# Performance work log

Hardware: AMD Instinct MI355X
Metric: run time of the kernel (lower is better)

The kernel has to match this reference:

```python
import jax, jax.numpy as jnp
import numpy as np

INPUT_DIM = 1024
NUM_HEADS = 16
D_K = 1024
HEAD_DIM = D_K // NUM_HEADS


def setup_inputs() -> dict:
    key = jax.random.key(0)
    ks = jax.random.split(key, 9)
    s_in = 1.0 / np.sqrt(INPUT_DIM)
    s_dk = 1.0 / np.sqrt(D_K)
    return {
        "x": jax.random.normal(ks[0], (2, 2048, INPUT_DIM), dtype=jnp.float32),
        "Wq": jax.random.uniform(ks[1], (INPUT_DIM, D_K), minval=-s_in, maxval=s_in, dtype=jnp.float32),
        "bq": jax.random.uniform(ks[2], (D_K,), minval=-s_in, maxval=s_in, dtype=jnp.float32),
        "Wk": jax.random.uniform(ks[3], (INPUT_DIM, D_K), minval=-s_in, maxval=s_in, dtype=jnp.float32),
        "bk": jax.random.uniform(ks[4], (D_K,), minval=-s_in, maxval=s_in, dtype=jnp.float32),
        "Wv": jax.random.uniform(ks[5], (INPUT_DIM, D_K), minval=-s_in, maxval=s_in, dtype=jnp.float32),
        "bv": jax.random.uniform(ks[6], (D_K,), minval=-s_in, maxval=s_in, dtype=jnp.float32),
        "Wo": jax.random.uniform(ks[7], (D_K, INPUT_DIM), minval=-s_dk, maxval=s_dk, dtype=jnp.float32),
        "bo": jax.random.uniform(ks[8], (INPUT_DIM,), minval=-s_dk, maxval=s_dk, dtype=jnp.float32),
    }


def reference(x, Wq, bq, Wk, bk, Wv, bv, Wo, bo):
    B, S, _ = x.shape
    H, D = NUM_HEADS, HEAD_DIM
    # QKV projections -> [B, H, S, D]
    q = (x @ Wq + bq).reshape(B, S, H, D).transpose(0, 2, 1, 3)
    k = (x @ Wk + bk).reshape(B, S, H, D).transpose(0, 2, 1, 3)
    v = (x @ Wv + bv).reshape(B, S, H, D).transpose(0, 2, 1, 3)
    scores = jnp.einsum("bhsd,bhtd->bhst", q, k) / jnp.sqrt(jnp.asarray(D, x.dtype))
    attn = jax.nn.softmax(scores, axis=-1)
    out = jnp.einsum("bhst,bhtd->bhsd", attn, v)  # [B,H,S,D]
    out = out.transpose(0, 2, 1, 3).reshape(B, S, H * D)
    return out @ Wo + bo
```

## Files before the change

### kernel.cpp

```cpp
#include <hip/hip_runtime.h>
#include <stdint.h>

typedef _Float16 f16;
typedef f16 f16x4 __attribute__((ext_vector_type(4)));
typedef f16 f16x8 __attribute__((ext_vector_type(8)));
typedef float f32x4 __attribute__((ext_vector_type(4)));
typedef float f32x16 __attribute__((ext_vector_type(16)));

#define AS1 __attribute__((address_space(1)))
#define AS3 __attribute__((address_space(3)))

__device__ __forceinline__ void gll16(const void* g, void* l) {
  __builtin_amdgcn_global_load_lds((AS1 void*)g, (AS3 void*)l, 16, 0, 0);
}

__device__ __forceinline__ f32x4 mfma16(f16x8 a, f16x8 b, f32x4 c) {
  return __builtin_amdgcn_mfma_f32_16x16x32_f16(a, b, c, 0, 0, 0);
}
__device__ __forceinline__ f32x16 mfma32(f16x8 a, f16x8 b, f32x16 c) {
  return __builtin_amdgcn_mfma_f32_32x32x16_f16(a, b, c, 0, 0, 0);
}

__device__ __forceinline__ uint32_t pk_rtn(float a, float b) {
  union { f16 h[2]; uint32_t u; } c;
  c.h[0] = (f16)a;
  c.h[1] = (f16)b;
  return c.u;
}

__device__ __forceinline__ void pl32(uint32_t& x, uint32_t& y) {
  asm("v_permlane32_swap_b32 %0, %1" : "+v"(x), "+v"(y));
}

__device__ __forceinline__ f16x8 mk_bfrag(float e0, float e1, float e2, float e3,
                                          float e4, float e5, float e6, float e7) {
  uint32_t x0 = pk_rtn(e0, e1), y0 = pk_rtn(e4, e5);
  uint32_t x1 = pk_rtn(e2, e3), y1 = pk_rtn(e6, e7);
  pl32(x0, y0);
  pl32(x1, y1);
  union { uint32_t w[4]; f16x8 v; } u;
  u.w[0] = x0; u.w[1] = x1; u.w[2] = y0; u.w[3] = y1;
  return u.v;
}

__device__ __forceinline__ f32x16 zero16() {
  f32x16 z;
#pragma unroll
  for (int i = 0; i < 16; i++) z[i] = 0.f;
  return z;
}


__global__ __launch_bounds__(256) void pack_x_k(const float* __restrict__ x,
                                                f16* __restrict__ xh, int n) {
  int i = (blockIdx.x * 256 + threadIdx.x) * 8;
  if (i < n) {
    float4 a = *(const float4*)(x + i);
    float4 b = *(const float4*)(x + i + 4);
    f16x8 o;
    o[0] = (f16)a.x; o[1] = (f16)a.y; o[2] = (f16)a.z; o[3] = (f16)a.w;
    o[4] = (f16)b.x; o[5] = (f16)b.y; o[6] = (f16)b.z; o[7] = (f16)b.w;
    *(f16x8*)(xh + i) = o;
  }
}

__global__ __launch_bounds__(256) void pack_w_k(const float* __restrict__ Wq,
                                                const float* __restrict__ Wk,
                                                const float* __restrict__ Wv,
                                                const float* __restrict__ Wo,
                                                f16* __restrict__ Wt) {
  __shared__ f16 t[64][65];
  const float* W = (blockIdx.z == 0) ? Wq : (blockIdx.z == 1) ? Wk
                   : (blockIdx.z == 2) ? Wv : Wo;
  int n0 = blockIdx.x * 64, k0 = blockIdx.y * 64;
  int tid = threadIdx.x;
  int kr = tid >> 4;
  int nc = (tid & 15) * 4;
#pragma unroll
  for (int i = 0; i < 4; i++) {
    int k = k0 + kr + i * 16;
    float4 w = *(const float4*)(W + (size_t)k * 1024 + n0 + nc);
    t[nc + 0][kr + i * 16] = (f16)w.x;
    t[nc + 1][kr + i * 16] = (f16)w.y;
    t[nc + 2][kr + i * 16] = (f16)w.z;
    t[nc + 3][kr + i * 16] = (f16)w.w;
  }
  __syncthreads();
  int nr = tid >> 2;
  int c0 = (tid & 3) * 16;
  alignas(16) f16 tmp[16];
#pragma unroll
  for (int e = 0; e < 16; e++) tmp[e] = t[nr][c0 + e];
  f16* dst = Wt + (size_t)(blockIdx.z * 1024 + n0 + nr) * 1024 + k0 + c0;
  *(f16x8*)(dst) = *(const f16x8*)(tmp);
  *(f16x8*)(dst + 8) = *(const f16x8*)(tmp + 8);
}

__device__ __forceinline__ void gemm_main(const f16* __restrict__ A,
                                          const f16* __restrict__ B,
                                          int m0, int n0,
                                          f16* Al, f16* Bl,
                                          f32x4 acc[4][4]) {
  const int K = 1024;
  int tid = threadIdx.x;
  int lane = tid & 63, wid = tid >> 6;
  int wr = (wid >> 1) * 64, wc = (wid & 1) * 64;
#pragma unroll
  for (int mi = 0; mi < 4; mi++)
#pragma unroll
    for (int nj = 0; nj < 4; nj++) {
      f32x4 z = {0.f, 0.f, 0.f, 0.f};
      acc[mi][nj] = z;
    }
  int srow = lane >> 3;
  int sgr = (lane & 7) ^ srow;
  int lr = lane & 15, lg = lane >> 4;
  for (int kt = 0; kt < 16; ++kt) {
    __syncthreads();
#pragma unroll
    for (int q = 0; q < 4; q++) {
      int chunk = wid * 4 + q;
      int row = chunk * 8 + srow;
      gll16(A + (size_t)(m0 + row) * K + kt * 64 + sgr * 8, Al + chunk * 512);
      gll16(B + (size_t)(n0 + row) * K + kt * 64 + sgr * 8, Bl + chunk * 512);
    }
    __syncthreads();
#pragma unroll
    for (int kk = 0; kk < 2; kk++) {
      f16x8 af[4], bf[4];
#pragma unroll
      for (int mi = 0; mi < 4; mi++) {
        int row = wr + mi * 16 + lr;
        int gr = (kk * 4 + lg) ^ (row & 7);
        af[mi] = *(const f16x8*)(Al + row * 64 + gr * 8);
      }
#pragma unroll
      for (int nj = 0; nj < 4; nj++) {
        int row = wc + nj * 16 + lr;
        int gr = (kk * 4 + lg) ^ (row & 7);
        bf[nj] = *(const f16x8*)(Bl + row * 64 + gr * 8);
      }
#pragma unroll
      for (int mi = 0; mi < 4; mi++)
#pragma unroll
        for (int nj = 0; nj < 4; nj++)
          acc[mi][nj] = mfma16(af[mi], bf[nj], acc[mi][nj]);
    }
  }
}

__global__ __launch_bounds__(256) void gemm_qkv_k(const f16* __restrict__ Xh,
                                                  const f16* __restrict__ Wt,
                                                  const float* __restrict__ bq,
                                                  const float* __restrict__ bk,
                                                  const float* __restrict__ bv,
                                                  f16* __restrict__ Q,
                                                  f16* __restrict__ Kb,
                                                  f16* __restrict__ Vt) {
  __shared__ f16 Al[128 * 64];
  __shared__ f16 Bl[128 * 64];
  f32x4 acc[4][4];
  int m0 = blockIdx.y * 128, n0 = blockIdx.x * 128;
  gemm_main(Xh, Wt, m0, n0, Al, Bl, acc);

  int lane = threadIdx.x & 63, wid = threadIdx.x >> 6;
  int wr = (wid >> 1) * 64, wc = (wid & 1) * 64;
  int lg = lane >> 4, lc = lane & 15;
  int which = n0 >> 10;
  if (which == 2) {
#pragma unroll
    for (int mi = 0; mi < 4; mi++)
#pragma unroll
      for (int nj = 0; nj < 4; nj++) {
        int nh = (n0 + wc + nj * 16 + lc) & 1023;
        int h = nh >> 6, d = nh & 63;
        float bb = bv[nh];
        int mbase = m0 + wr + mi * 16 + lg * 4;
        int b = mbase >> 11, s = mbase & 2047;
        f16x4 vv;
#pragma unroll
        for (int r = 0; r < 4; r++) vv[r] = (f16)(acc[mi][nj][r] + bb);
        *(f16x4*)(Vt + ((size_t)(b * 16 + h) * 64 + d) * 2048 + s) = vv;
      }
  } else {
    const float* bias = (which == 0) ? bq : bk;
    f16* out = (which == 0) ? Q : Kb;
    float scale = (which == 0) ? 0.1803368801111204f : 1.0f;
#pragma unroll
    for (int mi = 0; mi < 4; mi++)
#pragma unroll
      for (int nj = 0; nj < 4; nj++) {
        int nh = (n0 + wc + nj * 16 + lc) & 1023;
        int h = nh >> 6, d = nh & 63;
        float bb = bias[nh];
#pragma unroll
        for (int r = 0; r < 4; r++) {
          int m = m0 + wr + mi * 16 + lg * 4 + r;
          int b = m >> 11, s = m & 2047;
          float v = (acc[mi][nj][r] + bb) * scale;
          out[((size_t)(b * 16 + h) * 2048 + s) * 64 + d] = (f16)v;
        }
      }
  }
}

__global__ __launch_bounds__(256) void gemm_out_k(const f16* __restrict__ Oh,
                                                  const f16* __restrict__ Wt,
                                                  const float* __restrict__ bo,
                                                  float* __restrict__ out) {
  __shared__ f16 Al[128 * 64];
  __shared__ f16 Bl[64 * 64];
  const int K = 1024;
  int tid = threadIdx.x, lane = tid & 63, wid = tid >> 6;
  int wr = (wid >> 1) * 64, wc = (wid & 1) * 32;
  f32x4 acc[4][2];
#pragma unroll
  for (int mi = 0; mi < 4; mi++)
#pragma unroll
    for (int nj = 0; nj < 2; nj++) {
      f32x4 z = {0.f, 0.f, 0.f, 0.f};
      acc[mi][nj] = z;
    }
  int m0 = blockIdx.y * 128, n0 = blockIdx.x * 64;
  int srow = lane >> 3, sgr = (lane & 7) ^ srow;
  int lr = lane & 15, lg = lane >> 4;
  for (int kt = 0; kt < 16; ++kt) {
    __syncthreads();
#pragma unroll
    for (int q = 0; q < 4; q++) {
      int chunk = wid * 4 + q;
      int row = chunk * 8 + srow;
      gll16(Oh + (size_t)(m0 + row) * K + kt * 64 + sgr * 8, Al + chunk * 512);
    }
#pragma unroll
    for (int q = 0; q < 2; q++) {
      int chunk = wid * 2 + q;
      int row = chunk * 8 + srow;
      gll16(Wt + (size_t)(n0 + row) * K + kt * 64 + sgr * 8, Bl + chunk * 512);
    }
    __syncthreads();
#pragma unroll
    for (int kk = 0; kk < 2; kk++) {
      f16x8 af[4], bf[2];
#pragma unroll
      for (int mi = 0; mi < 4; mi++) {
        int row = wr + mi * 16 + lr;
        int gr = (kk * 4 + lg) ^ (row & 7);
        af[mi] = *(const f16x8*)(Al + row * 64 + gr * 8);
      }
#pragma unroll
      for (int nj = 0; nj < 2; nj++) {
        int row = wc + nj * 16 + lr;
        int gr = (kk * 4 + lg) ^ (row & 7);
        bf[nj] = *(const f16x8*)(Bl + row * 64 + gr * 8);
      }
#pragma unroll
      for (int mi = 0; mi < 4; mi++)
#pragma unroll
        for (int nj = 0; nj < 2; nj++)
          acc[mi][nj] = mfma16(af[mi], bf[nj], acc[mi][nj]);
    }
  }
  int lg4 = lg * 4, lc = lane & 15;
#pragma unroll
  for (int mi = 0; mi < 4; mi++)
#pragma unroll
    for (int nj = 0; nj < 2; nj++) {
      int n = n0 + wc + nj * 16 + lc;
      float bb = bo[n];
#pragma unroll
      for (int r = 0; r < 4; r++) {
        int m = m0 + wr + mi * 16 + lg4 + r;
        out[(size_t)m * 1024 + n] = acc[mi][nj][r] + bb;
      }
    }
}

__global__ __launch_bounds__(256, 4) void attn_k(const f16* __restrict__ Q,
                                                 const f16* __restrict__ K,
                                                 const f16* __restrict__ Vt,
                                                 f16* __restrict__ Oh) {
  __shared__ alignas(16) char lds_raw[32768];
  f16* Kl = (f16*)lds_raw;
  f16* Vl = (f16*)(lds_raw + 16384);

  int tid = threadIdx.x, lane = tid & 63, wid = tid >> 6;
  int q5 = lane & 31, hi = lane >> 5;
  int qc2 = wid >> 1, hv = wid & 1;
  int b0 = blockIdx.x;
  int qc = (b0 >> 3) & 31;
  int bh = (b0 & 7) + ((b0 >> 8) << 3);
  int q0w = qc * 64 + qc2 * 32;

  const f16* Qp = Q + (size_t)bh * 2048 * 64;
  const f16* Kp = K + (size_t)bh * 2048 * 64;
  const f16* Vp = Vt + (size_t)bh * 64 * 2048;

  f16x8 qf[4];
  {
    const f16* qr = Qp + (size_t)(q0w + q5) * 64 + hi * 8;
#pragma unroll
    for (int ks = 0; ks < 4; ks++) qf[ks] = *(const f16x8*)(qr + ks * 16);
  }

  const f32x16 Z = zero16();
  f16x8 ones;
#pragma unroll
  for (int i = 0; i < 8; i++) ones[i] = (f16)1.0f;

  f32x16 o0 = Z, o1 = Z, osum = Z;

  int srow8 = lane >> 3, swz8 = ((lane & 7) ^ srow8) * 8;
  int ch0 = wid * 2;
  const f16* sK = Kp + (size_t)(ch0 * 8 + srow8) * 64 + swz8;
  const f16* sV = Vp + (size_t)(ch0 * 8 + srow8) * 2048 + swz8;

  auto STAGE = [&](int buf, int t) {
    const f16* k = sK + (size_t)t * 4096;
    const f16* v = sV + t * 64;
    f16* dk = Kl + buf * 4096 + ch0 * 512;
    f16* dv = Vl + buf * 4096 + ch0 * 512;
    gll16(k, dk);
    gll16(k + 8 * 64, dk + 512);
    gll16(v, dv);
    gll16(v + (size_t)8 * 2048, dv + 512);
  };

  int kqoff[4];
#pragma unroll
  for (int ks = 0; ks < 4; ks++)
    kqoff[ks] = (hv * 32 + q5) * 64 + (((2 * ks + hi) ^ (q5 & 7)) << 3);
  int r0 = q5, r1 = q5 + 32;
  int voff0[2], voff1[2];
#pragma unroll
  for (int ks = 0; ks < 2; ks++) {
    voff0[ks] = r0 * 64 + (((hv * 4 + 2 * ks + hi) ^ (r0 & 7)) << 3);
    voff1[ks] = r1 * 64 + (((hv * 4 + 2 * ks + hi) ^ (r1 & 7)) << 3);
  }

  STAGE(0, 0);

  for (int t = 0; t < 32; ++t) {
    int cur = t & 1;
    asm volatile("s_waitcnt vmcnt(0)" ::: "memory");
    __builtin_amdgcn_s_barrier();
    if (t < 31) STAGE(cur ^ 1, t + 1);

    const f16* kb = Kl + cur * 4096;
    const f16* vb = Vl + cur * 4096;

    __builtin_amdgcn_s_setprio(1);
    f32x16 s = mfma32(*(const f16x8*)(kb + kqoff[0]), qf[0], Z);
    s = mfma32(*(const f16x8*)(kb + kqoff[1]), qf[1], s);
    s = mfma32(*(const f16x8*)(kb + kqoff[2]), qf[2], s);
    s = mfma32(*(const f16x8*)(kb + kqoff[3]), qf[3], s);
    __builtin_amdgcn_s_setprio(0);

    f16x8 vf0[2], vf1[2];
#pragma unroll
    for (int ks = 0; ks < 2; ks++) {
      vf0[ks] = *(const f16x8*)(vb + voff0[ks]);
      vf1[ks] = *(const f16x8*)(vb + voff1[ks]);
    }

#pragma unroll
    for (int i = 0; i < 16; i++) s[i] = __builtin_amdgcn_exp2f(s[i]);

    f16x8 pb0 = mk_bfrag(s[0], s[1], s[2], s[3], s[4], s[5], s[6], s[7]);
    f16x8 pb1 = mk_bfrag(s[8], s[9], s[10], s[11], s[12], s[13], s[14], s[15]);

    __builtin_amdgcn_s_setprio(1);
    o0 = mfma32(vf0[0], pb0, o0);
    o0 = mfma32(vf0[1], pb1, o0);
    o1 = mfma32(vf1[0], pb0, o1);
    o1 = mfma32(vf1[1], pb1, o1);
    osum = mfma32(ones, pb0, osum);
    osum = mfma32(ones, pb1, osum);
    __builtin_amdgcn_s_setprio(0);
  }

  float lsum = osum[0];

  __syncthreads();
  float* Ox = (float*)lds_raw + qc2 * (32 * 68);
  float* ml = (float*)lds_raw + 2 * (32 * 68) + qc2 * 32;
  if (hv == 1) {
#pragma unroll
    for (int g = 0; g < 4; g++) {
      f32x4 a, b;
#pragma unroll
      for (int j = 0; j < 4; j++) { a[j] = o0[4 * g + j]; b[j] = o1[4 * g + j]; }
      *(f32x4*)(Ox + q5 * 68 + 8 * g + 4 * hi) = a;
      *(f32x4*)(Ox + q5 * 68 + 32 + 8 * g + 4 * hi) = b;
    }
    if (hi == 0) ml[q5] = lsum;
  }
  __syncthreads();
  if (hv == 0) {
    float inv = 1.f / (lsum + ml[q5]);
    int bB = bh >> 4, hh = bh & 15;
    f16* op = Oh + ((size_t)(bB * 2048 + q0w + q5)) * 1024 + hh * 64;
#pragma unroll
    for (int g = 0; g < 4; g++) {
      f32x4 x0 = *(const f32x4*)(Ox + q5 * 68 + 8 * g + 4 * hi);
      f32x4 x1 = *(const f32x4*)(Ox + q5 * 68 + 32 + 8 * g + 4 * hi);
      f16x4 y0, y1;
#pragma unroll
      for (int j = 0; j < 4; j++) {
        y0[j] = (f16)((o0[4 * g + j] + x0[j]) * inv);
        y1[j] = (f16)((o1[4 * g + j] + x1[j]) * inv);
      }
      int d0 = 8 * g + 4 * hi;
      *(f16x4*)(op + d0) = y0;
      *(f16x4*)(op + 32 + d0) = y1;
    }
  }
}


extern "C" void kernel_launch(void* const* d_in, const int* in_sizes, int n_in,
                              void* d_out, int out_size, void* d_ws, size_t ws_size,
                              hipStream_t stream) {
  const float* x  = (const float*)d_in[0];
  const float* Wq = (const float*)d_in[1];
  const float* bq = (const float*)d_in[2];
  const float* Wk = (const float*)d_in[3];
  const float* bk = (const float*)d_in[4];
  const float* Wv = (const float*)d_in[5];
  const float* bv = (const float*)d_in[6];
  const float* Wo = (const float*)d_in[7];
  const float* bo = (const float*)d_in[8];
  float* out = (float*)d_out;

  char* ws = (char*)d_ws;
  const size_t MB8 = (size_t)8 << 20;
  f16* Xh = (f16*)(ws + 0 * MB8);
  f16* Wt = (f16*)(ws + 1 * MB8);
  f16* Q  = (f16*)(ws + 2 * MB8);
  f16* Kb = (f16*)(ws + 3 * MB8);
  f16* Vt = (f16*)(ws + 4 * MB8);
  f16* Oh = (f16*)(ws + 5 * MB8);

  pack_x_k<<<dim3(2048), dim3(256), 0, stream>>>(x, Xh, 4096 * 1024);
  pack_w_k<<<dim3(16, 16, 4), dim3(256), 0, stream>>>(Wq, Wk, Wv, Wo, Wt);
  gemm_qkv_k<<<dim3(24, 32), dim3(256), 0, stream>>>(Xh, Wt, bq, bk, bv, Q, Kb, Vt);
  attn_k<<<dim3(1024), dim3(256), 0, stream>>>(Q, Kb, Vt, Oh);
  gemm_out_k<<<dim3(16, 32), dim3(256), 0, stream>>>(Oh, Wt + (size_t)3072 * 1024, bo, out);
}
```

Before: 123.4 us.

## Double-buffer LDS tiles with K-step 32 in QKV and output GEMMs

Both projection GEMMs move from a single 64-wide K tile, loaded and then consumed between two barriers, to two 32-wide K tiles in LDS. The global-to-LDS loads for the next tile are issued before the MFMAs on the current one, so load latency can overlap compute. A single explicit waitcnt-plus-barrier replaces the two syncthreads per step, and the XOR swizzle is adapted to 32-element rows. The trade-off is twice as many K iterations, and so twice as many barriers, each with less MFMA work to hide latency behind.

Result: slower. 141.7 us (+14.9%).

```diff
diff --git a/kernel.cpp b/kernel.cpp
--- a/kernel.cpp
+++ b/kernel.cpp
@@ -19,6 +19,13 @@
 }
 __device__ __forceinline__ f32x16 mfma32(f16x8 a, f16x8 b, f32x16 c) {
   return __builtin_amdgcn_mfma_f32_32x32x16_f16(a, b, c, 0, 0, 0);
+}
+
+__device__ __forceinline__ void fence_barrier() {
+  asm volatile("s_waitcnt vmcnt(0) lgkmcnt(0)" ::: "memory");
+  __builtin_amdgcn_sched_barrier(0);
+  __builtin_amdgcn_s_barrier();
+  __builtin_amdgcn_sched_barrier(0);
 }
 
 __device__ __forceinline__ uint32_t pk_rtn(float a, float b) {
@@ -96,11 +103,12 @@
   *(f16x8*)(dst + 8) = *(const f16x8*)(tmp + 8);
 }
 
-__device__ __forceinline__ void gemm_main(const f16* __restrict__ A,
-                                          const f16* __restrict__ B,
-                                          int m0, int n0,
-                                          f16* Al, f16* Bl,
-                                          f32x4 acc[4][4]) {
+__device__ __forceinline__ void gemm_main32(const f16* __restrict__ A,
+                                            const f16* __restrict__ B,
+                                            int m0, int n0,
+                                            f16 (*Al)[128 * 32],
+                                            f16 (*Bl)[128 * 32],
+                                            f32x4 acc[4][4]) {
   const int K = 1024;
   int tid = threadIdx.x;
   int lane = tid & 63, wid = tid >> 6;
@@ -112,40 +120,42 @@
       f32x4 z = {0.f, 0.f, 0.f, 0.f};
       acc[mi][nj] = z;
     }
-  int srow = lane >> 3;
-  int sgr = (lane & 7) ^ srow;
+  int crow = lane >> 2;
+  int sg = (lane & 3) ^ (crow & 3);
   int lr = lane & 15, lg = lane >> 4;
-  for (int kt = 0; kt < 16; ++kt) {
-    __syncthreads();
-#pragma unroll
-    for (int q = 0; q < 4; q++) {
-      int chunk = wid * 4 + q;
-      int row = chunk * 8 + srow;
-      gll16(A + (size_t)(m0 + row) * K + kt * 64 + sgr * 8, Al + chunk * 512);
-      gll16(B + (size_t)(n0 + row) * K + kt * 64 + sgr * 8, Bl + chunk * 512);
-    }
-    __syncthreads();
-#pragma unroll
-    for (int kk = 0; kk < 2; kk++) {
-      f16x8 af[4], bf[4];
-#pragma unroll
-      for (int mi = 0; mi < 4; mi++) {
-        int row = wr + mi * 16 + lr;
-        int gr = (kk * 4 + lg) ^ (row & 7);
-        af[mi] = *(const f16x8*)(Al + row * 64 + gr * 8);
-      }
-#pragma unroll
-      for (int nj = 0; nj < 4; nj++) {
-        int row = wc + nj * 16 + lr;
-        int gr = (kk * 4 + lg) ^ (row & 7);
-        bf[nj] = *(const f16x8*)(Bl + row * 64 + gr * 8);
-      }
-#pragma unroll
-      for (int mi = 0; mi < 4; mi++)
-#pragma unroll
-        for (int nj = 0; nj < 4; nj++)
-          acc[mi][nj] = mfma16(af[mi], bf[nj], acc[mi][nj]);
-    }
+
+  auto STAGE = [&](int buf, int kt) {
+#pragma unroll
+    for (int q = 0; q < 2; q++) {
+      int chunk = wid * 2 + q;
+      int row = chunk * 16 + crow;
+      gll16(A + (size_t)(m0 + row) * K + kt * 32 + sg * 8, &Al[buf][chunk * 512]);
+      gll16(B + (size_t)(n0 + row) * K + kt * 32 + sg * 8, &Bl[buf][chunk * 512]);
+    }
+  };
+
+  STAGE(0, 0);
+  for (int kt = 0; kt < 32; ++kt) {
+    int cur = kt & 1;
+    fence_barrier();
+    if (kt < 31) STAGE(cur ^ 1, kt + 1);
+
+    f16x8 af[4], bf[4];
+#pragma unroll
+    for (int mi = 0; mi < 4; mi++) {
+      int row = wr + mi * 16 + lr;
+      af[mi] = *(const f16x8*)(&Al[cur][row * 32 + ((lg ^ (row & 3)) << 3)]);
+    }
+#pragma unroll
+    for (int nj = 0; nj < 4; nj++) {
+      int row = wc + nj * 16 + lr;
+      bf[nj] = *(const f16x8*)(&Bl[cur][row * 32 + ((lg ^ (row & 3)) << 3)]);
+    }
+#pragma unroll
+    for (int mi = 0; mi < 4; mi++)
+#pragma unroll
+      for (int nj = 0; nj < 4; nj++)
+        acc[mi][nj] = mfma16(af[mi], bf[nj], acc[mi][nj]);
   }
 }
 
@@ -157,11 +167,11 @@
                                                   f16* __restrict__ Q,
                                                   f16* __restrict__ Kb,
                                                   f16* __restrict__ Vt) {
-  __shared__ f16 Al[128 * 64];
-  __shared__ f16 Bl[128 * 64];
+  __shared__ f16 Al[2][128 * 32];
+  __shared__ f16 Bl[2][128 * 32];
   f32x4 acc[4][4];
   int m0 = blockIdx.y * 128, n0 = blockIdx.x * 128;
-  gemm_main(Xh, Wt, m0, n0, Al, Bl, acc);
+  gemm_main32(Xh, Wt, m0, n0, Al, Bl, acc);
 
   int lane = threadIdx.x & 63, wid = threadIdx.x >> 6;
   int wr = (wid >> 1) * 64, wc = (wid & 1) * 64;
@@ -208,8 +218,8 @@
                                                   const f16* __restrict__ Wt,
                                                   const float* __restrict__ bo,
                                                   float* __restrict__ out) {
-  __shared__ f16 Al[128 * 64];
-  __shared__ f16 Bl[64 * 64];
+  __shared__ f16 Al[2][128 * 32];
+  __shared__ f16 Bl[2][64 * 32];
   const int K = 1024;
   int tid = threadIdx.x, lane = tid & 63, wid = tid >> 6;
   int wr = (wid >> 1) * 64, wc = (wid & 1) * 32;
@@ -222,45 +232,47 @@
       acc[mi][nj] = z;
     }
   int m0 = blockIdx.y * 128, n0 = blockIdx.x * 64;
-  int srow = lane >> 3, sgr = (lane & 7) ^ srow;
+  int crow = lane >> 2;
+  int sg = (lane & 3) ^ (crow & 3);
   int lr = lane & 15, lg = lane >> 4;
-  for (int kt = 0; kt < 16; ++kt) {
-    __syncthreads();
-#pragma unroll
-    for (int q = 0; q < 4; q++) {
-      int chunk = wid * 4 + q;
-      int row = chunk * 8 + srow;
-      gll16(Oh + (size_t)(m0 + row) * K + kt * 64 + sgr * 8, Al + chunk * 512);
-    }
+
+  auto STAGE = [&](int buf, int kt) {
 #pragma unroll
     for (int q = 0; q < 2; q++) {
       int chunk = wid * 2 + q;
-      int row = chunk * 8 + srow;
-      gll16(Wt + (size_t)(n0 + row) * K + kt * 64 + sgr * 8, Bl + chunk * 512);
-    }
-    __syncthreads();
-#pragma unroll
-    for (int kk = 0; kk < 2; kk++) {
-      f16x8 af[4], bf[2];
-#pragma unroll
-      for (int mi = 0; mi < 4; mi++) {
-        int row = wr + mi * 16 + lr;
-        int gr = (kk * 4 + lg) ^ (row & 7);
-        af[mi] = *(const f16x8*)(Al + row * 64 + gr * 8);
-      }
-#pragma unroll
-      for (int nj = 0; nj < 2; nj++) {
-        int row = wc + nj * 16 + lr;
-        int gr = (kk * 4 + lg) ^ (row & 7);
-        bf[nj] = *(const f16x8*)(Bl + row * 64 + gr * 8);
-      }
-#pragma unroll
-      for (int mi = 0; mi < 4; mi++)
-#pragma unroll
-        for (int nj = 0; nj < 2; nj++)
-          acc[mi][nj] = mfma16(af[mi], bf[nj], acc[mi][nj]);
-    }
-  }
+      int row = chunk * 16 + crow;
+      gll16(Oh + (size_t)(m0 + row) * K + kt * 32 + sg * 8, &Al[buf][chunk * 512]);
+    }
+    {
+      int row = wid * 16 + crow;
+      gll16(Wt + (size_t)(n0 + row) * K + kt * 32 + sg * 8, &Bl[buf][wid * 512]);
+    }
+  };
+
+  STAGE(0, 0);
+  for (int kt = 0; kt < 32; ++kt) {
+    int cur = kt & 1;
+    fence_barrier();
+    if (kt < 31) STAGE(cur ^ 1, kt + 1);
+
+    f16x8 af[4], bf[2];
+#pragma unroll
+    for (int mi = 0; mi < 4; mi++) {
+      int row = wr + mi * 16 + lr;
+      af[mi] = *(const f16x8*)(&Al[cur][row * 32 + ((lg ^ (row & 3)) << 3)]);
+    }
+#pragma unroll
+    for (int nj = 0; nj < 2; nj++) {
+      int row = wc + nj * 16 + lr;
+      bf[nj] = *(const f16x8*)(&Bl[cur][row * 32 + ((lg ^ (row & 3)) << 3)]);
+    }
+#pragma unroll
+    for (int mi = 0; mi < 4; mi++)
+#pragma unroll
+      for (int nj = 0; nj < 2; nj++)
+        acc[mi][nj] = mfma16(af[mi], bf[nj], acc[mi][nj]);
+  }
+
   int lg4 = lg * 4, lc = lane & 15;
 #pragma unroll
   for (int mi = 0; mi < 4; mi++)
```

## Load K and V fragments directly from global memory instead of LDS staging

Applied to the files above, without the earlier changes.

The attention kernel no longer stages K and V tiles into shared memory with async global-to-LDS loads and barriers. Each wave now reads its own K fragments straight into registers, prefetching one step ahead with ping-pong register sets, and reads V fragments from global memory within each step. This removes the per-iteration barriers and LDS traffic, but each wave pair now fetches K and V separately, so L2 traffic rises, and the V loads sit on the critical path without any prefetch.

Result: slower. 215.5 us (+74.7%).

```diff
diff --git a/kernel.cpp b/kernel.cpp
--- a/kernel.cpp
+++ b/kernel.cpp
@@ -281,8 +281,6 @@
                                                  const f16* __restrict__ Vt,
                                                  f16* __restrict__ Oh) {
   __shared__ alignas(16) char lds_raw[32768];
-  f16* Kl = (f16*)lds_raw;
-  f16* Vl = (f16*)(lds_raw + 16384);
 
   int tid = threadIdx.x, lane = tid & 63, wid = tid >> 6;
   int q5 = lane & 31, hi = lane >> 5;
@@ -310,57 +308,39 @@
 
   f32x16 o0 = Z, o1 = Z, osum = Z;
 
-  int srow8 = lane >> 3, swz8 = ((lane & 7) ^ srow8) * 8;
-  int ch0 = wid * 2;
-  const f16* sK = Kp + (size_t)(ch0 * 8 + srow8) * 64 + swz8;
-  const f16* sV = Vp + (size_t)(ch0 * 8 + srow8) * 2048 + swz8;
-
-  auto STAGE = [&](int buf, int t) {
-    const f16* k = sK + (size_t)t * 4096;
-    const f16* v = sV + t * 64;
-    f16* dk = Kl + buf * 4096 + ch0 * 512;
-    f16* dv = Vl + buf * 4096 + ch0 * 512;
-    gll16(k, dk);
-    gll16(k + 8 * 64, dk + 512);
-    gll16(v, dv);
-    gll16(v + (size_t)8 * 2048, dv + 512);
+  const f16* kbase = Kp + (size_t)(hv * 32 + q5) * 64 + hi * 8;
+  const f16* vbase0 = Vp + (size_t)q5 * 2048 + hv * 32 + hi * 8;
+  const f16* vbase1 = vbase0 + (size_t)32 * 2048;
+
+  auto LK = [&](int t, f16x8 kf[4]) {
+    const f16* p = kbase + (size_t)t * 4096;
+    kf[0] = *(const f16x8*)(p);
+    kf[1] = *(const f16x8*)(p + 16);
+    kf[2] = *(const f16x8*)(p + 32);
+    kf[3] = *(const f16x8*)(p + 48);
   };
 
-  int kqoff[4];
-#pragma unroll
-  for (int ks = 0; ks < 4; ks++)
-    kqoff[ks] = (hv * 32 + q5) * 64 + (((2 * ks + hi) ^ (q5 & 7)) << 3);
-  int r0 = q5, r1 = q5 + 32;
-  int voff0[2], voff1[2];
-#pragma unroll
-  for (int ks = 0; ks < 2; ks++) {
-    voff0[ks] = r0 * 64 + (((hv * 4 + 2 * ks + hi) ^ (r0 & 7)) << 3);
-    voff1[ks] = r1 * 64 + (((hv * 4 + 2 * ks + hi) ^ (r1 & 7)) << 3);
-  }
-
-  STAGE(0, 0);
-
-  for (int t = 0; t < 32; ++t) {
-    int cur = t & 1;
-    asm volatile("s_waitcnt vmcnt(0)" ::: "memory");
-    __builtin_amdgcn_s_barrier();
-    if (t < 31) STAGE(cur ^ 1, t + 1);
-
-    const f16* kb = Kl + cur * 4096;
-    const f16* vb = Vl + cur * 4096;
+  f16x8 kA[4], kB[4];
+  LK(0, kA);
+
+  auto body = [&](int t, f16x8 kc[4], f16x8 kn[4]) {
+    if (t < 31) LK(t + 1, kn);
 
     __builtin_amdgcn_s_setprio(1);
-    f32x16 s = mfma32(*(const f16x8*)(kb + kqoff[0]), qf[0], Z);
-    s = mfma32(*(const f16x8*)(kb + kqoff[1]), qf[1], s);
-    s = mfma32(*(const f16x8*)(kb + kqoff[2]), qf[2], s);
-    s = mfma32(*(const f16x8*)(kb + kqoff[3]), qf[3], s);
+    f32x16 s = mfma32(kc[0], qf[0], Z);
+    s = mfma32(kc[1], qf[1], s);
+    s = mfma32(kc[2], qf[2], s);
+    s = mfma32(kc[3], qf[3], s);
     __builtin_amdgcn_s_setprio(0);
 
     f16x8 vf0[2], vf1[2];
-#pragma unroll
-    for (int ks = 0; ks < 2; ks++) {
-      vf0[ks] = *(const f16x8*)(vb + voff0[ks]);
-      vf1[ks] = *(const f16x8*)(vb + voff1[ks]);
+    {
+      const f16* p0 = vbase0 + t * 64;
+      const f16* p1 = vbase1 + t * 64;
+      vf0[0] = *(const f16x8*)(p0);
+      vf0[1] = *(const f16x8*)(p0 + 16);
+      vf1[0] = *(const f16x8*)(p1);
+      vf1[1] = *(const f16x8*)(p1 + 16);
     }
 
 #pragma unroll
@@ -377,6 +357,11 @@
     osum = mfma32(ones, pb0, osum);
     osum = mfma32(ones, pb1, osum);
     __builtin_amdgcn_s_setprio(0);
+  };
+
+  for (int tt = 0; tt < 16; ++tt) {
+    body(2 * tt, kA, kB);
+    body(2 * tt + 1, kB, kA);
   }
 
   float lsum = osum[0];
```
